# Performance work log

Measured on AMD Instinct MI355X. Metric: run time of the kernel, lower is better.

Reference implementation:

```python
import jax, jax.numpy as jnp
import numpy as np

B, N, D, H = 4, 8192, 1024, 16
C = D // H  # head dim = 64
EPS = 1e-6


def setup_inputs() -> dict:
    key = jax.random.key(0)
    ks = jax.random.split(key, 8)
    sc = 0.02
    return {
        "q": jax.random.normal(ks[0], (B, N, D), jnp.float32),
        "k": jax.random.normal(ks[1], (B, N, D), jnp.float32),
        "v": jax.random.normal(ks[2], (B, N, D), jnp.float32),
        "Wq": jax.random.normal(ks[3], (D, D), jnp.float32) * sc,
        "Wk": jax.random.normal(ks[4], (D, D), jnp.float32) * sc,
        "Wv": jax.random.normal(ks[5], (D, D), jnp.float32) * sc,
        "Wproj": jax.random.normal(ks[6], (D, D), jnp.float32) * sc,
        "focusing_factor": jnp.asarray(3.0, jnp.float32),
    }


def _to_heads(x):
    # b n (h c) -> (b h) n c
    return x.reshape(B, N, H, C).transpose(0, 2, 1, 3).reshape(B * H, N, C)


def reference(q, k, v, Wq, Wk, Wv, Wproj, focusing_factor):
    # projections (torch Linear: x @ W.T, no bias)
    qp = q @ Wq.T
    kp = k @ Wk.T
    vp = v @ Wv.T

    def feature_map(x):
        # |GELU(x)| + eps, then focused renormalization:
        # softmax(focusing_factor * log(f)) * mean(f)
        f = jnp.abs(jax.nn.gelu(x, approximate=False)) + EPS
        f_norm = f.mean(axis=-1, keepdims=True)
        return jax.nn.softmax(jnp.log(f) * focusing_factor, axis=-1) * f_norm

    qf = feature_map(qp)
    kf = feature_map(kp)

    qh = _to_heads(qf)  # [B*H, N, C]
    kh = _to_heads(kf)
    vh = _to_heads(vp)

    k_mean = kh.mean(axis=1)  # [B*H, C]
    z_inv = jnp.einsum('bnd,bd->bn', qh, k_mean) + EPS  # [B*H, N]

    # (k/sqrt(N))^T (v/sqrt(N)) == (k^T v)/N
    kv = jnp.einsum('bnc,bnd->bcd', kh, vh) / N  # [B*H, C, C]
    y = jnp.einsum('bic,bcd->bid', qh, kv) / z_inv[..., None]  # [B*H, N, C]

    y = y.reshape(B, H, N, C).transpose(0, 2, 1, 3).reshape(B, N, D)
    return y @ Wproj.T
```

## Files before the change

kernel.cpp:

```cpp
#include <hip/hip_runtime.h>

using f16 = _Float16;
typedef __attribute__((ext_vector_type(4))) _Float16 f16x4;
typedef __attribute__((ext_vector_type(8))) _Float16 f16x8;
typedef __attribute__((ext_vector_type(4))) float f32x4;

#define DEVI __device__ __forceinline__

namespace {

constexpr int BB = 4;
constexpr int NN = 8192;
constexpr int DD = 1024;
constexpr int MTOT = BB * NN;
constexpr float FSCALE = 64.0f;
constexpr float ZCONST = 64.0f * 64.0f * (8192.0f * 1e-6f);
constexpr float SC = 4096.0f;

DEVI void gl16(const void* g, void* l) {
  __builtin_amdgcn_global_load_lds(
      (__attribute__((address_space(1))) void*)(void*)g,
      (__attribute__((address_space(3))) void*)l, 16, 0, 0);
}

DEVI float wsum(float v) {
#pragma unroll
  for (int m = 32; m > 0; m >>= 1) v += __shfl_xor(v, m, 64);
  return v;
}

struct CastArgs {
  const float* src[4];
  f16* dst[4];
  int n4[4];
};

__global__ __launch_bounds__(256) void cast_kernel(CastArgs a) {
  const int z = blockIdx.y;
  const float4* __restrict__ s = (const float4*)a.src[z];
  f16x4* __restrict__ d = (f16x4*)a.dst[z];
  const int n4 = a.n4[z];
  for (int i = blockIdx.x * blockDim.x + threadIdx.x; i < n4;
       i += gridDim.x * blockDim.x) {
    float4 f = s[i];
    f16x4 o = {(f16)f.x, (f16)f.y, (f16)f.z, (f16)f.w};
    d[i] = o;
  }
}

struct Gemm3f {
  const float* A[3];
  const f16* Bt[3];
  f16* C[3];
};
struct GemmZf {
  const f16* A;
  const f16* M;
  const float* colsum;
  float* C;
};

#define GEMM_PREAMBLE()                                                      \
  constexpr int K = DD;                                                      \
  constexpr int N = DD;                                                      \
  constexpr int NKT = K / 64;                                                \
  const int nx = gridDim.x;                                                  \
  int lin = blockIdx.y * nx + blockIdx.x;                                    \
  const int cpx = (gridDim.y * nx) >> 3;                                     \
  lin = (lin & 7) * cpx + (lin >> 3);                                        \
  const size_t row0 = (size_t)(lin / nx) * 256;                              \
  const size_t col0 = (size_t)(lin % nx) * 256;                              \
  const int tid = threadIdx.x, lane = tid & 63, wv = tid >> 6;               \
  const int wm = wv >> 2, wn = wv & 3;                                       \
  const int fr = lane & 15, f7 = lane & 7, kq = lane >> 4;                   \
  const int srow = wv * 8 + (lane >> 3);                                     \
  const int ssw = (lane & 7) ^ ((lane >> 3) & 7);                            \
  const int c0e = (kq ^ f7) * 8;

__global__ __launch_bounds__(512, 2) void gemm256_fa(Gemm3f P) {
  GEMM_PREAMBLE()
  const int z = blockIdx.z;
  const float* __restrict__ A = P.A[z];
  const f16* __restrict__ Bt = P.Bt[z];
  f16* __restrict__ C = P.C[z];

  __shared__ __align__(16) f16 LA[2][2][8192];
  __shared__ __align__(16) f16 LB[2][2][8192];

  auto stageB = [&](int kts, int half) {
    const f16* src = Bt + (col0 + half * 128 + srow) * K + kts * 64 + ssw * 8;
    f16* dst = &LB[kts & 1][half][wv * 512];
#pragma unroll
    for (int c = 0; c < 2; ++c) gl16(src + (size_t)c * 64 * K, dst + c * 4096);
  };

  const int ar = tid >> 2;
  const int ac2 = (tid & 3) * 2;
  auto loadA = [&](int kts, float4* r) {
#pragma unroll
    for (int half = 0; half < 2; ++half) {
      const float* src = A + (row0 + half * 128 + ar) * (size_t)K + kts * 64;
#pragma unroll
      for (int c = 0; c < 2; ++c) {
        r[half * 4 + 2 * c + 0] = *(const float4*)(src + (ac2 + c) * 8);
        r[half * 4 + 2 * c + 1] = *(const float4*)(src + (ac2 + c) * 8 + 4);
      }
    }
  };
  auto writeA = [&](int kts, const float4* r) {
#pragma unroll
    for (int half = 0; half < 2; ++half) {
      f16* base = &LA[kts & 1][half][ar * 64];
#pragma unroll
      for (int c = 0; c < 2; ++c) {
        const float4 lo = r[half * 4 + 2 * c], hi = r[half * 4 + 2 * c + 1];
        f16x8 o = {(f16)lo.x, (f16)lo.y, (f16)lo.z, (f16)lo.w,
                   (f16)hi.x, (f16)hi.y, (f16)hi.z, (f16)hi.w};
        *(f16x8*)&base[((ac2 + c) ^ (ar & 7)) * 8] = o;
      }
    }
  };

  f32x4 acc[8][4];
#pragma unroll
  for (int i = 0; i < 8; ++i)
#pragma unroll
    for (int j = 0; j < 4; ++j) acc[i][j] = f32x4{0.f, 0.f, 0.f, 0.f};

  float4 ra[8];
  loadA(0, ra);
  stageB(0, 0); stageB(0, 1);
  asm volatile("s_waitcnt vmcnt(0)" ::: "memory");
  writeA(0, ra);
  asm volatile("s_waitcnt lgkmcnt(0)" ::: "memory");
  loadA(1, ra);
  __builtin_amdgcn_s_barrier();

  for (int kt = 0; kt < NKT; ++kt) {
    const int buf = kt & 1;
    const f16* Ah = LA[buf][wm];
    const f16* Bh = &LB[buf][wn >> 1][(wn & 1) * 4096];
    f16x8 a0[8], a1[8], b0[4], b1[4];

#pragma unroll
    for (int mi = 0; mi < 8; ++mi)
      a0[mi] = *(const f16x8*)&Ah[(mi * 16 + fr) * 64 + c0e];
#pragma unroll
    for (int ni = 0; ni < 4; ++ni)
      b0[ni] = *(const f16x8*)&Bh[(ni * 16 + fr) * 64 + c0e];
    if (kt + 1 < NKT) stageB(kt + 1, 0);
    __builtin_amdgcn_s_barrier();
    asm volatile("s_waitcnt lgkmcnt(0)" ::: "memory");
    __builtin_amdgcn_sched_barrier(0);
    __builtin_amdgcn_s_setprio(1);
#pragma unroll
    for (int mi = 0; mi < 4; ++mi)
#pragma unroll
      for (int ni = 0; ni < 4; ++ni)
        acc[mi][ni] = __builtin_amdgcn_mfma_f32_16x16x32_f16(
            a0[mi], b0[ni], acc[mi][ni], 0, 0, 0);
    __builtin_amdgcn_s_setprio(0);
    __builtin_amdgcn_s_barrier();

#pragma unroll
    for (int mi = 0; mi < 8; ++mi)
      a1[mi] = *(const f16x8*)&Ah[(mi * 16 + fr) * 64 + (c0e ^ 32)];
    if (kt + 1 < NKT) stageB(kt + 1, 1);
    __builtin_amdgcn_s_barrier();
    asm volatile("s_waitcnt lgkmcnt(0)" ::: "memory");
    __builtin_amdgcn_sched_barrier(0);
    __builtin_amdgcn_s_setprio(1);
#pragma unroll
    for (int mi = 4; mi < 8; ++mi)
#pragma unroll
      for (int ni = 0; ni < 4; ++ni)
        acc[mi][ni] = __builtin_amdgcn_mfma_f32_16x16x32_f16(
            a0[mi], b0[ni], acc[mi][ni], 0, 0, 0);
    __builtin_amdgcn_s_setprio(0);
    __builtin_amdgcn_s_barrier();

#pragma unroll
    for (int ni = 0; ni < 4; ++ni)
      b1[ni] = *(const f16x8*)&Bh[(ni * 16 + fr) * 64 + (c0e ^ 32)];
    __builtin_amdgcn_s_barrier();
    asm volatile("s_waitcnt lgkmcnt(0)" ::: "memory");
    __builtin_amdgcn_sched_barrier(0);
    __builtin_amdgcn_s_setprio(1);
#pragma unroll
    for (int mi = 0; mi < 4; ++mi)
#pragma unroll
      for (int ni = 0; ni < 4; ++ni)
        acc[mi][ni] = __builtin_amdgcn_mfma_f32_16x16x32_f16(
            a1[mi], b1[ni], acc[mi][ni], 0, 0, 0);
    __builtin_amdgcn_s_setprio(0);
    __builtin_amdgcn_s_barrier();

    __builtin_amdgcn_s_setprio(1);
#pragma unroll
    for (int mi = 4; mi < 8; ++mi)
#pragma unroll
      for (int ni = 0; ni < 4; ++ni)
        acc[mi][ni] = __builtin_amdgcn_mfma_f32_16x16x32_f16(
            a1[mi], b1[ni], acc[mi][ni], 0, 0, 0);
    __builtin_amdgcn_s_setprio(0);
    asm volatile("s_waitcnt vmcnt(0)" ::: "memory");
    __builtin_amdgcn_sched_barrier(0);
    if (kt + 1 < NKT) {
      writeA(kt + 1, ra);
      asm volatile("s_waitcnt lgkmcnt(0)" ::: "memory");
      if (kt + 2 < NKT) loadA(kt + 2, ra);
    }
    __builtin_amdgcn_s_barrier();
  }

#pragma unroll
  for (int mi = 0; mi < 8; ++mi)
#pragma unroll
    for (int ni = 0; ni < 4; ++ni) {
      const size_t colv = col0 + wn * 64 + ni * 16 + fr;
#pragma unroll
      for (int r = 0; r < 4; ++r) {
        const size_t rowv = row0 + wm * 128 + mi * 16 + (lane >> 4) * 4 + r;
        C[rowv * N + colv] = (f16)acc[mi][ni][r];
      }
    }
}

__global__ __launch_bounds__(512, 2) void gemm256_zf(GemmZf P) {
  GEMM_PREAMBLE()
  const f16* __restrict__ A = P.A;
  float* __restrict__ C = P.C;
  const int batch = (int)(row0 >> 13);
  const f16* __restrict__ Bt = P.M + (size_t)batch * DD * DD;

  __shared__ __align__(16) f16 LA[2][2][8192];
  __shared__ __align__(16) f16 LB[2][2][8192];

  auto stageB = [&](int kts, int half) {
    const f16* src = Bt + (col0 + half * 128 + srow) * K + kts * 64 + ssw * 8;
    f16* dst = &LB[kts & 1][half][wv * 512];
#pragma unroll
    for (int c = 0; c < 2; ++c) gl16(src + (size_t)c * 64 * K, dst + c * 4096);
  };

  const int ar = tid >> 2;
  const int ac2 = (tid & 3) * 2;
  f16x8 ra[4];
  float csr[16];

  auto loadA = [&](int kts) {
#pragma unroll
    for (int half = 0; half < 2; ++half) {
      const f16* src =
          A + (row0 + half * 128 + ar) * (size_t)K + kts * 64 + ac2 * 8;
      ra[half * 2 + 0] = *(const f16x8*)(src);
      ra[half * 2 + 1] = *(const f16x8*)(src + 8);
    }
  };
  auto loadCS = [&](int head) {
    const float* cs = P.colsum + ((batch << 4) + head) * 64 + ac2 * 8;
#pragma unroll
    for (int j = 0; j < 16; ++j) csr[j] = cs[j];
  };
  auto writeA = [&](int kts) {
#pragma unroll
    for (int half = 0; half < 2; ++half) {
      float xv[16];
      float dot = 0.f;
#pragma unroll
      for (int c = 0; c < 2; ++c)
#pragma unroll
        for (int j = 0; j < 8; ++j) {
          const float x = (float)ra[half * 2 + c][j];
          xv[c * 8 + j] = x;
          dot += x * csr[c * 8 + j];
        }
      dot += __shfl_xor(dot, 1, 64);
      dot += __shfl_xor(dot, 2, 64);
      const float s = SC / (dot + ZCONST);
      f16* base = &LA[kts & 1][half][ar * 64];
#pragma unroll
      for (int c = 0; c < 2; ++c) {
        f16x8 o;
#pragma unroll
        for (int j = 0; j < 8; ++j) o[j] = (f16)(xv[c * 8 + j] * s);
        *(f16x8*)&base[((ac2 + c) ^ (ar & 7)) * 8] = o;
      }
    }
  };

  f32x4 acc[8][4];
#pragma unroll
  for (int i = 0; i < 8; ++i)
#pragma unroll
    for (int j = 0; j < 4; ++j) acc[i][j] = f32x4{0.f, 0.f, 0.f, 0.f};

  loadA(0);
  stageB(0, 0); stageB(0, 1);
  loadCS(0);
  asm volatile("s_waitcnt vmcnt(0)" ::: "memory");
  writeA(0);
  asm volatile("s_waitcnt lgkmcnt(0)" ::: "memory");
  loadA(1);
  loadCS(1);
  __builtin_amdgcn_s_barrier();

  for (int kt = 0; kt < NKT; ++kt) {
    const int buf = kt & 1;
    const f16* Ah = LA[buf][wm];
    const f16* Bh = &LB[buf][wn >> 1][(wn & 1) * 4096];
    f16x8 a0[8], a1[8], b0[4], b1[4];

#pragma unroll
    for (int mi = 0; mi < 8; ++mi)
      a0[mi] = *(const f16x8*)&Ah[(mi * 16 + fr) * 64 + c0e];
#pragma unroll
    for (int ni = 0; ni < 4; ++ni)
      b0[ni] = *(const f16x8*)&Bh[(ni * 16 + fr) * 64 + c0e];
    if (kt + 1 < NKT) stageB(kt + 1, 0);
    __builtin_amdgcn_s_barrier();
    asm volatile("s_waitcnt lgkmcnt(0)" ::: "memory");
    __builtin_amdgcn_sched_barrier(0);
    __builtin_amdgcn_s_setprio(1);
#pragma unroll
    for (int mi = 0; mi < 4; ++mi)
#pragma unroll
      for (int ni = 0; ni < 4; ++ni)
        acc[mi][ni] = __builtin_amdgcn_mfma_f32_16x16x32_f16(
            a0[mi], b0[ni], acc[mi][ni], 0, 0, 0);
    __builtin_amdgcn_s_setprio(0);
    __builtin_amdgcn_s_barrier();

#pragma unroll
    for (int mi = 0; mi < 8; ++mi)
      a1[mi] = *(const f16x8*)&Ah[(mi * 16 + fr) * 64 + (c0e ^ 32)];
    if (kt + 1 < NKT) stageB(kt + 1, 1);
    __builtin_amdgcn_s_barrier();
    asm volatile("s_waitcnt lgkmcnt(0)" ::: "memory");
    __builtin_amdgcn_sched_barrier(0);
    __builtin_amdgcn_s_setprio(1);
#pragma unroll
    for (int mi = 4; mi < 8; ++mi)
#pragma unroll
      for (int ni = 0; ni < 4; ++ni)
        acc[mi][ni] = __builtin_amdgcn_mfma_f32_16x16x32_f16(
            a0[mi], b0[ni], acc[mi][ni], 0, 0, 0);
    __builtin_amdgcn_s_setprio(0);
    __builtin_amdgcn_s_barrier();

#pragma unroll
    for (int ni = 0; ni < 4; ++ni)
      b1[ni] = *(const f16x8*)&Bh[(ni * 16 + fr) * 64 + (c0e ^ 32)];
    __builtin_amdgcn_s_barrier();
    asm volatile("s_waitcnt lgkmcnt(0)" ::: "memory");
    __builtin_amdgcn_sched_barrier(0);
    __builtin_amdgcn_s_setprio(1);
#pragma unroll
    for (int mi = 0; mi < 4; ++mi)
#pragma unroll
      for (int ni = 0; ni < 4; ++ni)
        acc[mi][ni] = __builtin_amdgcn_mfma_f32_16x16x32_f16(
            a1[mi], b1[ni], acc[mi][ni], 0, 0, 0);
    __builtin_amdgcn_s_setprio(0);
    __builtin_amdgcn_s_barrier();

    __builtin_amdgcn_s_setprio(1);
#pragma unroll
    for (int mi = 4; mi < 8; ++mi)
#pragma unroll
      for (int ni = 0; ni < 4; ++ni)
        acc[mi][ni] = __builtin_amdgcn_mfma_f32_16x16x32_f16(
            a1[mi], b1[ni], acc[mi][ni], 0, 0, 0);
    __builtin_amdgcn_s_setprio(0);
    asm volatile("s_waitcnt vmcnt(0)" ::: "memory");
    __builtin_amdgcn_sched_barrier(0);
    if (kt + 1 < NKT) {
      writeA(kt + 1);
      asm volatile("s_waitcnt lgkmcnt(0)" ::: "memory");
      if (kt + 2 < NKT) { loadA(kt + 2); loadCS(kt + 2); }
    }
    __builtin_amdgcn_s_barrier();
  }

#pragma unroll
  for (int mi = 0; mi < 8; ++mi)
#pragma unroll
    for (int ni = 0; ni < 4; ++ni) {
      const size_t colv = col0 + wn * 64 + ni * 16 + fr;
#pragma unroll
      for (int r = 0; r < 4; ++r) {
        const size_t rowv = row0 + wm * 128 + mi * 16 + (lane >> 4) * 4 + r;
        C[rowv * N + colv] = acc[mi][ni][r];
      }
    }
}

__global__ __launch_bounds__(256) void feature_kernel(
    const f16* __restrict__ qp, const f16* __restrict__ kp,
    f16* __restrict__ qf, f16* __restrict__ kf, const float* __restrict__ ffp) {
  const int lane = threadIdx.x & 63;
  const size_t row = (size_t)blockIdx.x * 4 + (threadIdx.x >> 6);
  const bool isq = (blockIdx.y == 0);
  const f16* __restrict__ src = isq ? qp : kp;
  f16* __restrict__ dst = isq ? qf : kf;
  const float ff = ffp[0];

  const f16x8* p = (const f16x8*)(src + row * DD + lane * 16);
  f16x8 v0 = p[0], v1 = p[1];

  float f0[16];
  float ps = 0.f;
#pragma unroll
  for (int j = 0; j < 16; ++j) {
    const float x = (float)(j < 8 ? v0[j] : v1[j - 8]);
    const float ax = fabsf(x) * 0.70710678118654752f;
    const float tt = 1.0f / (1.0f + 0.3275911f * ax);
    const float poly =
        tt * (0.254829592f +
              tt * (-0.284496736f +
                    tt * (1.421413741f +
                          tt * (-1.453152027f + tt * 1.061405429f))));
    const float erfv = 1.0f - poly * __expf(-ax * ax);
    const float g = 0.5f * x * (1.0f + copysignf(erfv, x));
    const float fv = fabsf(g) + 1e-6f;
    f0[j] = fv;
    ps += fv;
  }
  const float fsum = wsum(ps);

  float e[16];
  float es = 0.f;
#pragma unroll
  for (int j = 0; j < 16; ++j) {
    e[j] = __expf(ff * __logf(f0[j]));
    es += e[j];
  }
  const float esum = wsum(es);

  const float scale = fsum * (1.0f / 1024.0f) / esum * FSCALE;
  f16x8 o0, o1;
#pragma unroll
  for (int j = 0; j < 8; ++j) {
    o0[j] = (f16)(e[j] * scale);
    o1[j] = (f16)(e[j + 8] * scale);
  }
  f16x8* q = (f16x8*)(dst + row * DD + lane * 16);
  q[0] = o0;
  q[1] = o1;
}

__global__ __launch_bounds__(256) void kv_kernel(
    const f16* __restrict__ kf, const f16* __restrict__ vp,
    float* __restrict__ kvsum, float* __restrict__ colsum) {
  const int bh = blockIdx.x;
  const int b = bh >> 4, h = bh & 15;
  const int tid = threadIdx.x, lane = tid & 63, wave = tid >> 6;
  __shared__ __align__(16) f16 kt[32 * 64];
  __shared__ __align__(16) f16 vt[32 * 64];
  __shared__ float csred[4][64];

  f32x4 acc[4];
#pragma unroll
  for (int ni = 0; ni < 4; ++ni) acc[ni] = f32x4{0.f, 0.f, 0.f, 0.f};
  float cpart = 0.f;

  const int srow = wave * 8 + (lane >> 3);
  const int scol = (lane & 7) * 8;
  const int colbase = h * 64;
  const int n0base = blockIdx.y * 512;

  for (int n0 = n0base; n0 < n0base + 512; n0 += 32) {
    const size_t gofs = ((size_t)(b * NN + n0 + srow)) * DD + colbase + scol;
    gl16(kf + gofs, &kt[wave * 512]);
    gl16(vp + gofs, &vt[wave * 512]);
    __syncthreads();
    {
      const int c = tid & 63;
      const int r0 = (tid >> 6) * 8;
#pragma unroll
      for (int rr = 0; rr < 8; ++rr) cpart += (float)kt[(r0 + rr) * 64 + c];
    }
    f16x8 a, bfr[4];
#pragma unroll
    for (int j = 0; j < 8; ++j)
      a[j] = kt[((lane >> 4) * 8 + j) * 64 + wave * 16 + (lane & 15)];
#pragma unroll
    for (int ni = 0; ni < 4; ++ni)
#pragma unroll
      for (int j = 0; j < 8; ++j)
        bfr[ni][j] = vt[((lane >> 4) * 8 + j) * 64 + ni * 16 + (lane & 15)];
#pragma unroll
    for (int ni = 0; ni < 4; ++ni)
      acc[ni] = __builtin_amdgcn_mfma_f32_16x16x32_f16(a, bfr[ni], acc[ni], 0, 0, 0);
    __syncthreads();
  }
#pragma unroll
  for (int ni = 0; ni < 4; ++ni)
#pragma unroll
    for (int r = 0; r < 4; ++r) {
      const int c = wave * 16 + (lane >> 4) * 4 + r;
      const int d = ni * 16 + (lane & 15);
      atomicAdd(&kvsum[(size_t)bh * 4096 + c * 64 + d], acc[ni][r]);
    }
  csred[tid >> 6][tid & 63] = cpart;
  __syncthreads();
  if (tid < 64)
    atomicAdd(&colsum[bh * 64 + tid],
              csred[0][tid] + csred[1][tid] + csred[2][tid] + csred[3][tid]);
}

__global__ __launch_bounds__(256) void mprep_kernel(
    const float* __restrict__ kvsum, const float* __restrict__ Wp,
    f16* __restrict__ M) {
  const int bh = blockIdx.x, b = bh >> 4, h = bh & 15;
  const int tid = threadIdx.x;
  __shared__ float kvs[64 * 64];
#pragma unroll
  for (int j = 0; j < 4; ++j)
    ((float4*)kvs)[tid * 4 + j] =
        ((const float4*)(kvsum + (size_t)bh * 4096))[tid * 4 + j];
  __syncthreads();

  const int dp = blockIdx.y * 256 + tid;
  float wr[64];
#pragma unroll
  for (int j = 0; j < 16; ++j)
    *(float4*)&wr[j * 4] =
        *(const float4*)(Wp + (size_t)dp * DD + h * 64 + j * 4);

  f16 out[64];
#pragma unroll 4
  for (int c = 0; c < 64; ++c) {
    float s = 0.f;
#pragma unroll
    for (int d = 0; d < 64; ++d) s += kvs[c * 64 + d] * wr[d];
    out[c] = (f16)(s * (1.0f / SC));
  }
  f16* dst = M + (size_t)b * DD * DD + (size_t)dp * DD + h * 64;
#pragma unroll
  for (int j = 0; j < 8; ++j) ((f16x8*)dst)[j] = ((f16x8*)out)[j];
}

}

extern "C" void kernel_launch(void* const* d_in, const int* in_sizes, int n_in,
                              void* d_out, int out_size, void* d_ws, size_t ws_size,
                              hipStream_t stream) {
  const float* q = (const float*)d_in[0];
  const float* k = (const float*)d_in[1];
  const float* v = (const float*)d_in[2];
  const float* Wq = (const float*)d_in[3];
  const float* Wk = (const float*)d_in[4];
  const float* Wv = (const float*)d_in[5];
  const float* Wp = (const float*)d_in[6];
  const float* ffp = (const float*)d_in[7];

  char* w = (char*)d_ws;
  size_t off = 0;
  auto alloc = [&](size_t b) {
    void* p = (void*)(w + off);
    off += (b + 255) & ~(size_t)255;
    return p;
  };
  const size_t big = (size_t)MTOT * DD * sizeof(f16);
  f16* qp16 = (f16*)alloc(big);
  f16* kp16 = (f16*)alloc(big);
  f16* vp16 = (f16*)alloc(big);
  f16* qf  = (f16*)alloc(big);
  f16* kf  = (f16*)alloc(big);
  f16* M   = (f16*)alloc((size_t)BB * DD * DD * sizeof(f16));
  f16* Wq16 = (f16*)alloc((size_t)DD * DD * 2);
  f16* Wk16 = (f16*)alloc((size_t)DD * DD * 2);
  f16* Wv16 = (f16*)alloc((size_t)DD * DD * 2);
  float* kvsum = (float*)alloc(64 * 64 * 64 * sizeof(float));
  float* colsum = (float*)alloc(64 * 64 * sizeof(float));
  if (off > ws_size) return;

  CastArgs ca{};
  ca.src[0] = Wq; ca.dst[0] = Wq16; ca.n4[0] = DD * DD / 4;
  ca.src[1] = Wk; ca.dst[1] = Wk16; ca.n4[1] = DD * DD / 4;
  ca.src[2] = Wv; ca.dst[2] = Wv16; ca.n4[2] = DD * DD / 4;
  cast_kernel<<<dim3(128, 3), 256, 0, stream>>>(ca);
  hipMemsetAsync(kvsum, 0, 64 * 64 * 64 * sizeof(float) + 64 * 64 * sizeof(float),
                 stream);

  Gemm3f gp{};
  gp.A[0] = q; gp.Bt[0] = Wq16; gp.C[0] = qp16;
  gp.A[1] = k; gp.Bt[1] = Wk16; gp.C[1] = kp16;
  gp.A[2] = v; gp.Bt[2] = Wv16; gp.C[2] = vp16;
  gemm256_fa<<<dim3(DD / 256, MTOT / 256, 3), 512, 0, stream>>>(gp);

  feature_kernel<<<dim3(MTOT / 4, 2), 256, 0, stream>>>(qp16, kp16, qf, kf, ffp);

  kv_kernel<<<dim3(64, 16), 256, 0, stream>>>(kf, vp16, kvsum, colsum);

  mprep_kernel<<<dim3(64, 4), 256, 0, stream>>>(kvsum, Wp, M);

  GemmZf gz{};
  gz.A = qf; gz.M = M; gz.colsum = colsum; gz.C = (float*)d_out;
  gemm256_zf<<<dim3(DD / 256, MTOT / 256, 1), 512, 0, stream>>>(gz);
}
```

Baseline: 599.8 us.

## Move z-normalization into q feature kernel; stream GEMM A tiles via LDS DMA

Splits the feature kernel into separate k and q kernels. The q kernel now runs after kv_kernel, computes the per-head z-normalization dot with colsum and pre-scales its output. The final GEMM can then stage its A operand straight into LDS with async global_load_lds instead of loading into registers, rescaling and writing to LDS each k-step. This removes VALU and register-staging work from the GEMM's main loop and lets A prefetch two steps ahead, at the cost of an extra sequential launch and an extra barrier per iteration.

After: 605.8 us. About the same (+1.0%).

```diff
diff --git a/kernel.cpp b/kernel.cpp
--- a/kernel.cpp
+++ b/kernel.cpp
@@ -53,10 +53,9 @@
   const f16* Bt[3];
   f16* C[3];
 };
-struct GemmZf {
+struct GemmM {
   const f16* A;
   const f16* M;
-  const float* colsum;
   float* C;
 };
 
@@ -226,16 +225,22 @@
     }
 }
 
-__global__ __launch_bounds__(512, 2) void gemm256_zf(GemmZf P) {
+__global__ __launch_bounds__(512, 2) void gemm256_m(GemmM P) {
   GEMM_PREAMBLE()
   const f16* __restrict__ A = P.A;
-  float* __restrict__ C = P.C;
   const int batch = (int)(row0 >> 13);
   const f16* __restrict__ Bt = P.M + (size_t)batch * DD * DD;
+  float* __restrict__ C = P.C;
 
   __shared__ __align__(16) f16 LA[2][2][8192];
   __shared__ __align__(16) f16 LB[2][2][8192];
 
+  auto stageA = [&](int kts, int half) {
+    const f16* src = A + (row0 + half * 128 + srow) * K + kts * 64 + ssw * 8;
+    f16* dst = &LA[kts & 1][half][wv * 512];
+#pragma unroll
+    for (int c = 0; c < 2; ++c) gl16(src + (size_t)c * 64 * K, dst + c * 4096);
+  };
   auto stageB = [&](int kts, int half) {
     const f16* src = Bt + (col0 + half * 128 + srow) * K + kts * 64 + ssw * 8;
     f16* dst = &LB[kts & 1][half][wv * 512];
@@ -243,66 +248,15 @@
     for (int c = 0; c < 2; ++c) gl16(src + (size_t)c * 64 * K, dst + c * 4096);
   };
 
-  const int ar = tid >> 2;
-  const int ac2 = (tid & 3) * 2;
-  f16x8 ra[4];
-  float csr[16];
-
-  auto loadA = [&](int kts) {
-#pragma unroll
-    for (int half = 0; half < 2; ++half) {
-      const f16* src =
-          A + (row0 + half * 128 + ar) * (size_t)K + kts * 64 + ac2 * 8;
-      ra[half * 2 + 0] = *(const f16x8*)(src);
-      ra[half * 2 + 1] = *(const f16x8*)(src + 8);
-    }
-  };
-  auto loadCS = [&](int head) {
-    const float* cs = P.colsum + ((batch << 4) + head) * 64 + ac2 * 8;
-#pragma unroll
-    for (int j = 0; j < 16; ++j) csr[j] = cs[j];
-  };
-  auto writeA = [&](int kts) {
-#pragma unroll
-    for (int half = 0; half < 2; ++half) {
-      float xv[16];
-      float dot = 0.f;
-#pragma unroll
-      for (int c = 0; c < 2; ++c)
-#pragma unroll
-        for (int j = 0; j < 8; ++j) {
-          const float x = (float)ra[half * 2 + c][j];
-          xv[c * 8 + j] = x;
-          dot += x * csr[c * 8 + j];
-        }
-      dot += __shfl_xor(dot, 1, 64);
-      dot += __shfl_xor(dot, 2, 64);
-      const float s = SC / (dot + ZCONST);
-      f16* base = &LA[kts & 1][half][ar * 64];
-#pragma unroll
-      for (int c = 0; c < 2; ++c) {
-        f16x8 o;
-#pragma unroll
-        for (int j = 0; j < 8; ++j) o[j] = (f16)(xv[c * 8 + j] * s);
-        *(f16x8*)&base[((ac2 + c) ^ (ar & 7)) * 8] = o;
-      }
-    }
-  };
-
   f32x4 acc[8][4];
 #pragma unroll
   for (int i = 0; i < 8; ++i)
 #pragma unroll
     for (int j = 0; j < 4; ++j) acc[i][j] = f32x4{0.f, 0.f, 0.f, 0.f};
 
-  loadA(0);
-  stageB(0, 0); stageB(0, 1);
-  loadCS(0);
-  asm volatile("s_waitcnt vmcnt(0)" ::: "memory");
-  writeA(0);
-  asm volatile("s_waitcnt lgkmcnt(0)" ::: "memory");
-  loadA(1);
-  loadCS(1);
+  stageA(0, 0); stageA(0, 1); stageB(0, 0); stageB(0, 1);
+  stageA(1, 0); stageA(1, 1);
+  asm volatile("s_waitcnt vmcnt(4)" ::: "memory");
   __builtin_amdgcn_s_barrier();
 
   for (int kt = 0; kt < NKT; ++kt) {
@@ -317,7 +271,7 @@
 #pragma unroll
     for (int ni = 0; ni < 4; ++ni)
       b0[ni] = *(const f16x8*)&Bh[(ni * 16 + fr) * 64 + c0e];
-    if (kt + 1 < NKT) stageB(kt + 1, 0);
+    if (kt < NKT - 1) stageB(kt + 1, 0);
     __builtin_amdgcn_s_barrier();
     asm volatile("s_waitcnt lgkmcnt(0)" ::: "memory");
     __builtin_amdgcn_sched_barrier(0);
@@ -334,7 +288,7 @@
 #pragma unroll
     for (int mi = 0; mi < 8; ++mi)
       a1[mi] = *(const f16x8*)&Ah[(mi * 16 + fr) * 64 + (c0e ^ 32)];
-    if (kt + 1 < NKT) stageB(kt + 1, 1);
+    if (kt < NKT - 1) stageB(kt + 1, 1);
     __builtin_amdgcn_s_barrier();
     asm volatile("s_waitcnt lgkmcnt(0)" ::: "memory");
     __builtin_amdgcn_sched_barrier(0);
@@ -351,6 +305,7 @@
 #pragma unroll
     for (int ni = 0; ni < 4; ++ni)
       b1[ni] = *(const f16x8*)&Bh[(ni * 16 + fr) * 64 + (c0e ^ 32)];
+    if (kt < NKT - 2) stageA(kt + 2, 0);
     __builtin_amdgcn_s_barrier();
     asm volatile("s_waitcnt lgkmcnt(0)" ::: "memory");
     __builtin_amdgcn_sched_barrier(0);
@@ -364,6 +319,8 @@
     __builtin_amdgcn_s_setprio(0);
     __builtin_amdgcn_s_barrier();
 
+    if (kt < NKT - 2) stageA(kt + 2, 1);
+    __builtin_amdgcn_s_barrier();
     __builtin_amdgcn_s_setprio(1);
 #pragma unroll
     for (int mi = 4; mi < 8; ++mi)
@@ -372,13 +329,10 @@
         acc[mi][ni] = __builtin_amdgcn_mfma_f32_16x16x32_f16(
             a1[mi], b1[ni], acc[mi][ni], 0, 0, 0);
     __builtin_amdgcn_s_setprio(0);
-    asm volatile("s_waitcnt vmcnt(0)" ::: "memory");
-    __builtin_amdgcn_sched_barrier(0);
-    if (kt + 1 < NKT) {
-      writeA(kt + 1);
-      asm volatile("s_waitcnt lgkmcnt(0)" ::: "memory");
-      if (kt + 2 < NKT) { loadA(kt + 2); loadCS(kt + 2); }
-    }
+    if (kt < NKT - 2)
+      asm volatile("s_waitcnt vmcnt(4)" ::: "memory");
+    else
+      asm volatile("s_waitcnt vmcnt(0)" ::: "memory");
     __builtin_amdgcn_s_barrier();
   }
 
@@ -395,16 +349,8 @@
     }
 }
 
-__global__ __launch_bounds__(256) void feature_kernel(
-    const f16* __restrict__ qp, const f16* __restrict__ kp,
-    f16* __restrict__ qf, f16* __restrict__ kf, const float* __restrict__ ffp) {
-  const int lane = threadIdx.x & 63;
-  const size_t row = (size_t)blockIdx.x * 4 + (threadIdx.x >> 6);
-  const bool isq = (blockIdx.y == 0);
-  const f16* __restrict__ src = isq ? qp : kp;
-  f16* __restrict__ dst = isq ? qf : kf;
-  const float ff = ffp[0];
-
+DEVI void feature_core(const f16* __restrict__ src, size_t row, int lane,
+                       float ff, float* fv_out) {
   const f16x8* p = (const f16x8*)(src + row * DD + lane * 16);
   f16x8 v0 = p[0], v1 = p[1];
 
@@ -428,23 +374,66 @@
   }
   const float fsum = wsum(ps);
 
-  float e[16];
   float es = 0.f;
 #pragma unroll
   for (int j = 0; j < 16; ++j) {
-    e[j] = __expf(ff * __logf(f0[j]));
-    es += e[j];
+    f0[j] = __expf(ff * __logf(f0[j]));
+    es += f0[j];
   }
   const float esum = wsum(es);
 
   const float scale = fsum * (1.0f / 1024.0f) / esum * FSCALE;
+#pragma unroll
+  for (int j = 0; j < 16; ++j) fv_out[j] = f0[j] * scale;
+}
+
+__global__ __launch_bounds__(256) void feature_k_kernel(
+    const f16* __restrict__ kp, f16* __restrict__ kf,
+    const float* __restrict__ ffp) {
+  const int lane = threadIdx.x & 63;
+  const size_t row = (size_t)blockIdx.x * 4 + (threadIdx.x >> 6);
+  float fv[16];
+  feature_core(kp, row, lane, ffp[0], fv);
   f16x8 o0, o1;
 #pragma unroll
   for (int j = 0; j < 8; ++j) {
-    o0[j] = (f16)(e[j] * scale);
-    o1[j] = (f16)(e[j + 8] * scale);
-  }
-  f16x8* q = (f16x8*)(dst + row * DD + lane * 16);
+    o0[j] = (f16)fv[j];
+    o1[j] = (f16)fv[j + 8];
+  }
+  f16x8* q = (f16x8*)(kf + row * DD + lane * 16);
+  q[0] = o0;
+  q[1] = o1;
+}
+
+__global__ __launch_bounds__(256) void feature_q_kernel(
+    const f16* __restrict__ qp, const float* __restrict__ colsum,
+    f16* __restrict__ qs, const float* __restrict__ ffp) {
+  const int lane = threadIdx.x & 63;
+  const size_t row = (size_t)blockIdx.x * 4 + (threadIdx.x >> 6);
+  const int b = (int)(row >> 13);
+  float fv[16];
+  feature_core(qp, row, lane, ffp[0], fv);
+
+  const float* cs =
+      colsum + ((size_t)(b * 16 + (lane >> 2))) * 64 + (lane & 3) * 16;
+  float dot = 0.f;
+#pragma unroll
+  for (int j = 0; j < 4; ++j) {
+    const float4 c4 = *(const float4*)(cs + j * 4);
+    dot += fv[j * 4 + 0] * c4.x + fv[j * 4 + 1] * c4.y +
+           fv[j * 4 + 2] * c4.z + fv[j * 4 + 3] * c4.w;
+  }
+  dot += __shfl_xor(dot, 1, 64);
+  dot += __shfl_xor(dot, 2, 64);
+  const float s = SC / (dot + ZCONST);
+
+  f16x8 o0, o1;
+#pragma unroll
+  for (int j = 0; j < 8; ++j) {
+    o0[j] = (f16)(fv[j] * s);
+    o1[j] = (f16)(fv[j + 8] * s);
+  }
+  f16x8* q = (f16x8*)(qs + row * DD + lane * 16);
   q[0] = o0;
   q[1] = o1;
 }
@@ -566,8 +555,8 @@
   f16* qp16 = (f16*)alloc(big);
   f16* kp16 = (f16*)alloc(big);
   f16* vp16 = (f16*)alloc(big);
-  f16* qf  = (f16*)alloc(big);
   f16* kf  = (f16*)alloc(big);
+  f16* qs  = (f16*)alloc(big);
   f16* M   = (f16*)alloc((size_t)BB * DD * DD * sizeof(f16));
   f16* Wq16 = (f16*)alloc((size_t)DD * DD * 2);
   f16* Wk16 = (f16*)alloc((size_t)DD * DD * 2);
@@ -590,13 +579,15 @@
   gp.A[2] = v; gp.Bt[2] = Wv16; gp.C[2] = vp16;
   gemm256_fa<<<dim3(DD / 256, MTOT / 256, 3), 512, 0, stream>>>(gp);
 
-  feature_kernel<<<dim3(MTOT / 4, 2), 256, 0, stream>>>(qp16, kp16, qf, kf, ffp);
+  feature_k_kernel<<<dim3(MTOT / 4), 256, 0, stream>>>(kp16, kf, ffp);
 
   kv_kernel<<<dim3(64, 16), 256, 0, stream>>>(kf, vp16, kvsum, colsum);
 
   mprep_kernel<<<dim3(64, 4), 256, 0, stream>>>(kvsum, Wp, M);
 
-  GemmZf gz{};
-  gz.A = qf; gz.M = M; gz.colsum = colsum; gz.C = (float*)d_out;
-  gemm256_zf<<<dim3(DD / 256, MTOT / 256, 1), 512, 0, stream>>>(gz);
-}
+  feature_q_kernel<<<dim3(MTOT / 4), 256, 0, stream>>>(qp16, colsum, qs, ffp);
+
+  GemmM gm{};
+  gm.A = qs; gm.M = M; gm.C = (float*)d_out;
+  gemm256_m<<<dim3(DD / 256, MTOT / 256, 1), 512, 0, stream>>>(gm);
+}
```
